# Performance work log

Measured on AMD Instinct MI355X. Metric: run time of the kernel, lower is better.

Reference implementation:

```python
import jax, jax.numpy as jnp
import numpy as np

B, S, H = 4, 1024, 2048
NH, NKV = 32, 8
HD = H // NH  # 64
ROPE_THETA = 10000.0


def setup_inputs() -> dict:
    key = jax.random.key(0)
    ks = jax.random.split(key, 6)
    x = jax.random.normal(ks[0], (B, S, H), dtype=jnp.float32)
    # rotary tables: cos/sin of shape [B, S, HD] (duplicated half-dim layout)
    inv_freq = 1.0 / (ROPE_THETA ** (jnp.arange(0, HD, 2, dtype=jnp.float32) / HD))  # [HD/2]
    t = jnp.arange(S, dtype=jnp.float32)
    freqs = jnp.outer(t, inv_freq)                      # [S, HD/2]
    emb = jnp.concatenate([freqs, freqs], axis=-1)      # [S, HD]
    cos = jnp.broadcast_to(jnp.cos(emb), (B, S, HD))
    sin = jnp.broadcast_to(jnp.sin(emb), (B, S, HD))
    # additive causal mask [B, 1, S, S]
    causal = jnp.where(jnp.arange(S)[:, None] >= jnp.arange(S)[None, :], 0.0, -1e9).astype(jnp.float32)
    attention_mask = jnp.broadcast_to(causal[None, None], (B, 1, S, S))
    scale = 0.02
    Wq = jax.random.normal(ks[1], (H, NH * HD), dtype=jnp.float32) * scale
    Wk = jax.random.normal(ks[2], (H, NKV * HD), dtype=jnp.float32) * scale
    Wv = jax.random.normal(ks[3], (H, NKV * HD), dtype=jnp.float32) * scale
    Wo = jax.random.normal(ks[4], (NH * HD, H), dtype=jnp.float32) * scale
    return {"x": x, "cos": cos, "sin": sin, "attention_mask": attention_mask,
            "Wq": Wq, "Wk": Wk, "Wv": Wv, "Wo": Wo}


def _rotate_half(t):
    h = t.shape[-1] // 2
    return jnp.concatenate([-t[..., h:], t[..., :h]], axis=-1)


def reference(x, cos, sin, attention_mask, Wq, Wk, Wv, Wo):
    b, s, _ = x.shape
    q = (x @ Wq).reshape(b, s, NH, HD).transpose(0, 2, 1, 3)    # [B,NH,S,HD]
    k = (x @ Wk).reshape(b, s, NKV, HD).transpose(0, 2, 1, 3)   # [B,NKV,S,HD]
    v = (x @ Wv).reshape(b, s, NKV, HD).transpose(0, 2, 1, 3)
    c = cos[:, None]  # [B,1,S,HD]
    sn = sin[:, None]
    q = q * c + _rotate_half(q) * sn
    k = k * c + _rotate_half(k) * sn
    n_rep = NH // NKV
    k = jnp.repeat(k, n_rep, axis=1)  # [B,NH,S,HD]
    v = jnp.repeat(v, n_rep, axis=1)
    scaling = HD ** -0.5
    aw = jnp.einsum('bhqd,bhkd->bhqk', q, k) * scaling + attention_mask
    aw = jax.nn.softmax(aw, axis=-1)                            # [B,NH,S,S]
    out = jnp.einsum('bhqk,bhkd->bhqd', aw, v)                  # [B,NH,S,HD]
    out = out.transpose(0, 2, 1, 3).reshape(b, s, NH * HD) @ Wo  # [B,S,H]
    return out, aw
```

## Files before the change

### kernel.cpp

```cpp
#include <hip/hip_runtime.h>
#include <hip/hip_bf16.h>

#define NHQ 32
#define NKV 8
#define SEQ 1024
#define BATCH 4
#define HDIM 2048

typedef short bf16x8 __attribute__((ext_vector_type(8)));
typedef short short4v __attribute__((ext_vector_type(4)));
typedef float f32x4 __attribute__((ext_vector_type(4)));

__device__ __forceinline__ short f2bf(float f) {
  unsigned u = __builtin_bit_cast(unsigned, f);
  u += 0x7fff + ((u >> 16) & 1);
  return (short)(u >> 16);
}
__device__ __forceinline__ float bf2f(short s) {
  unsigned u = ((unsigned)(unsigned short)s) << 16;
  return __builtin_bit_cast(float, u);
}
__device__ __forceinline__ void gl2lds16(const void* g, void* l) {
  __builtin_amdgcn_global_load_lds(
      (const __attribute__((address_space(1))) unsigned int*)g,
      (__attribute__((address_space(3))) unsigned int*)l, 16, 0, 0);
}

__global__ __launch_bounds__(256) void convx_k(
    const float* __restrict__ x, short* __restrict__ xb)
{
  long i = ((long)blockIdx.x * 256 + threadIdx.x) * 4;
  float4 v = *(const float4*)(x + i);
  short4v o = {f2bf(v.x), f2bf(v.y), f2bf(v.z), f2bf(v.w)};
  *(short4v*)(xb + i) = o;
}

__global__ __launch_bounds__(256) void wtrans_k(
    const float* __restrict__ W, short* __restrict__ WT, int K, int N)
{
  __shared__ float t[64][65];
  int k0 = blockIdx.y * 64, n0 = blockIdx.x * 64;
  int r = threadIdx.x >> 4, c = (threadIdx.x & 15) * 4;
#pragma unroll
  for (int it = 0; it < 4; ++it) {
    float4 v = *(const float4*)(W + (long)(k0 + r + it * 16) * N + n0 + c);
    t[c + 0][r + it * 16] = v.x;
    t[c + 1][r + it * 16] = v.y;
    t[c + 2][r + it * 16] = v.z;
    t[c + 3][r + it * 16] = v.w;
  }
  __syncthreads();
  int wr = threadIdx.x >> 2, wc = (threadIdx.x & 3) * 16;
#pragma unroll
  for (int u = 0; u < 4; ++u) {
    short4v o = {f2bf(t[wr][wc + u * 4 + 0]), f2bf(t[wr][wc + u * 4 + 1]),
                 f2bf(t[wr][wc + u * 4 + 2]), f2bf(t[wr][wc + u * 4 + 3])};
    *(short4v*)&WT[(long)(n0 + wr) * K + k0 + wc + u * 4] = o;
  }
}

__global__ __launch_bounds__(256) void gemm_k(
    const short* __restrict__ A, const short* __restrict__ BT,
    void* __restrict__ C, int M, int N, int K, int mode, int nheads)
{
  __shared__ short smA[128 * 32];
  __shared__ short smB[128 * 32];
  const int tid = threadIdx.x;
  const int lane = tid & 63, w = tid >> 6;
  const int wr = w >> 1, wc = w & 1;
  const int lm = lane & 15, lk = lane >> 4;
  const int row0 = blockIdx.y * 128, col0 = blockIdx.x * 128;
  const int c0 = tid, c1 = tid + 256;

  const short* Ab = A + (long)row0 * K;
  const short* Bb = BT + (long)col0 * K;

  f32x4 acc[4][4] = {};

  for (int k0 = 0; k0 < K; k0 += 32) {
    gl2lds16(Ab + (long)(c0 >> 2) * K + k0 + (c0 & 3) * 8, &smA[c0 * 8]);
    gl2lds16(Ab + (long)(c1 >> 2) * K + k0 + (c1 & 3) * 8, &smA[c1 * 8]);
    gl2lds16(Bb + (long)(c0 >> 2) * K + k0 + (c0 & 3) * 8, &smB[c0 * 8]);
    gl2lds16(Bb + (long)(c1 >> 2) * K + k0 + (c1 & 3) * 8, &smB[c1 * 8]);
    __syncthreads();
    bf16x8 af[4], bf[4];
#pragma unroll
    for (int i = 0; i < 4; ++i)
      af[i] = *(const bf16x8*)&smA[(wr * 64 + i * 16 + lm) * 32 + lk * 8];
#pragma unroll
    for (int j = 0; j < 4; ++j)
      bf[j] = *(const bf16x8*)&smB[(wc * 64 + j * 16 + lm) * 32 + lk * 8];
#pragma unroll
    for (int i = 0; i < 4; ++i)
#pragma unroll
      for (int j = 0; j < 4; ++j)
        acc[i][j] = __builtin_amdgcn_mfma_f32_16x16x32_bf16(af[i], bf[j], acc[i][j], 0, 0, 0);
    __syncthreads();
  }

#pragma unroll
  for (int i = 0; i < 4; ++i) {
    int grow = row0 + wr * 64 + i * 16 + lk * 4;
#pragma unroll
    for (int j = 0; j < 4; ++j) {
      int gcol = col0 + wc * 64 + j * 16 + lm;
      if (mode == 0) {
        float* Co = (float*)C;
#pragma unroll
        for (int r = 0; r < 4; ++r)
          Co[(long)(grow + r) * N + gcol] = acc[i][j][r];
      } else if (mode == 1) {
        short* Co = (short*)C;
        int h = gcol >> 6, d = gcol & 63;
#pragma unroll
        for (int r = 0; r < 4; ++r) {
          int row = grow + r;
          int b = row >> 10, s = row & 1023;
          Co[((long)(b * nheads + h) * SEQ + s) * 64 + d] = f2bf(acc[i][j][r]);
        }
      } else {
        short* Co = (short*)C;
        int kvh = gcol >> 6, d = gcol & 63;
        int b = grow >> 10, s0 = grow & 1023;
        short4v o = {f2bf(acc[i][j][0]), f2bf(acc[i][j][1]),
                     f2bf(acc[i][j][2]), f2bf(acc[i][j][3])};
        *(short4v*)&Co[((long)(b * NKV + kvh) * 64 + d) * SEQ + s0] = o;
      }
    }
  }
}

__global__ __launch_bounds__(64) void rope_k(
    short* __restrict__ t, const float* __restrict__ cs,
    const float* __restrict__ sn, int nheads)
{
  long row = blockIdx.x;
  int d = threadIdx.x;
  int s = (int)(row & 1023);
  int b = (int)(row / ((long)nheads << 10));
  float v = bf2f(t[row * 64 + d]);
  float p = __shfl_xor(v, 32);
  float rh = (d < 32) ? -p : p;
  long ci = ((long)(b << 10) + s) * 64 + d;
  t[row * 64 + d] = f2bf(v * cs[ci] + rh * sn[ci]);
}

__global__ __launch_bounds__(256) void fattn_k(
    const short* __restrict__ Qb, const short* __restrict__ Kb,
    const short* __restrict__ Vt, float* __restrict__ aw,
    short* __restrict__ ctxb)
{
  __shared__ short Pl[4][32 * 72];
  const int bh = blockIdx.y;
  const int h = bh & 31, b = bh >> 5;
  const int q0 = blockIdx.x * 128;
  const int tid = threadIdx.x;
  const int lane = tid & 63, wv = tid >> 6;
  const int lm = lane & 15, lk = lane >> 4;

  const short* Qp = Qb + ((long)bh << 16);
  const short* Kp = Kb + ((long)(b * NKV + (h >> 2)) << 16);
  const short* Vp = Vt + ((long)(b * NKV + (h >> 2)) << 16);
  float* awb = aw + ((long)bh << 20);

  const int nch = (q0 >> 6) + 2;
  const int zc = nch * 64;

  if (zc < SEQ) {
    float4 z4 = make_float4(0.f, 0.f, 0.f, 0.f);
    for (int r = wv; r < 128; r += 4)
      for (int c = zc + lane * 4; c < SEQ; c += 256)
        *(float4*)(awb + (long)(q0 + r) * SEQ + c) = z4;
  }

  bf16x8 qa[2][2];
#pragma unroll
  for (int i = 0; i < 2; ++i)
#pragma unroll
    for (int hf = 0; hf < 2; ++hf)
      qa[i][hf] = *(const bf16x8*)(Qp + (long)(q0 + wv * 32 + i * 16 + lm) * 64 + hf * 32 + lk * 8);

  float m[2][4], l[2][4];
#pragma unroll
  for (int i = 0; i < 2; ++i)
#pragma unroll
    for (int r = 0; r < 4; ++r) { m[i][r] = -3.0e38f; l[i][r] = 0.f; }

  for (int ch = 0; ch < nch; ++ch) {
    const int k0c = ch * 64;
    bf16x8 kb[4][2];
#pragma unroll
    for (int j = 0; j < 4; ++j)
#pragma unroll
      for (int hf = 0; hf < 2; ++hf)
        kb[j][hf] = *(const bf16x8*)(Kp + (long)(k0c + j * 16 + lm) * 64 + hf * 32 + lk * 8);
    f32x4 s[2][4] = {};
#pragma unroll
    for (int i = 0; i < 2; ++i)
#pragma unroll
      for (int j = 0; j < 4; ++j) {
        s[i][j] = __builtin_amdgcn_mfma_f32_16x16x32_bf16(qa[i][0], kb[j][0], s[i][j], 0, 0, 0);
        s[i][j] = __builtin_amdgcn_mfma_f32_16x16x32_bf16(qa[i][1], kb[j][1], s[i][j], 0, 0, 0);
      }
#pragma unroll
    for (int i = 0; i < 2; ++i)
#pragma unroll
      for (int r = 0; r < 4; ++r) {
        const int qi = q0 + wv * 32 + i * 16 + lk * 4 + r;
        float cm = -3.0e38f;
#pragma unroll
        for (int j = 0; j < 4; ++j) {
          float sv = s[i][j][r] * 0.125f;
          cm = (qi >= k0c + j * 16 + lm) ? fmaxf(cm, sv) : cm;
        }
#pragma unroll
        for (int off = 1; off <= 8; off <<= 1) cm = fmaxf(cm, __shfl_xor(cm, off));
        float mn = fmaxf(m[i][r], cm);
        float sum = 0.f;
#pragma unroll
        for (int j = 0; j < 4; ++j) {
          float sv = s[i][j][r] * 0.125f;
          sum += (qi >= k0c + j * 16 + lm) ? __expf(sv - mn) : 0.f;
        }
#pragma unroll
        for (int off = 1; off <= 8; off <<= 1) sum += __shfl_xor(sum, off);
        l[i][r] = l[i][r] * __expf(m[i][r] - mn) + sum;
        m[i][r] = mn;
      }
  }
#pragma unroll
  for (int i = 0; i < 2; ++i)
#pragma unroll
    for (int r = 0; r < 4; ++r) l[i][r] = 1.f / l[i][r];

  f32x4 oacc[2][4] = {};
  short* Pw = Pl[wv];
  for (int ch = 0; ch < nch; ++ch) {
    const int k0c = ch * 64;
    bf16x8 kb[4][2];
#pragma unroll
    for (int j = 0; j < 4; ++j)
#pragma unroll
      for (int hf = 0; hf < 2; ++hf)
        kb[j][hf] = *(const bf16x8*)(Kp + (long)(k0c + j * 16 + lm) * 64 + hf * 32 + lk * 8);
    f32x4 s[2][4] = {};
#pragma unroll
    for (int i = 0; i < 2; ++i)
#pragma unroll
      for (int j = 0; j < 4; ++j) {
        s[i][j] = __builtin_amdgcn_mfma_f32_16x16x32_bf16(qa[i][0], kb[j][0], s[i][j], 0, 0, 0);
        s[i][j] = __builtin_amdgcn_mfma_f32_16x16x32_bf16(qa[i][1], kb[j][1], s[i][j], 0, 0, 0);
      }
#pragma unroll
    for (int i = 0; i < 2; ++i)
#pragma unroll
      for (int j = 0; j < 4; ++j)
#pragma unroll
        for (int r = 0; r < 4; ++r) {
          const int qi = q0 + wv * 32 + i * 16 + lk * 4 + r;
          const int ki = k0c + j * 16 + lm;
          float p = (qi >= ki) ? __expf(s[i][j][r] * 0.125f - m[i][r]) * l[i][r] : 0.f;
          awb[(long)qi * SEQ + ki] = p;
          Pw[(i * 16 + lk * 4 + r) * 72 + j * 16 + lm] = f2bf(p);
        }
    __syncthreads();
#pragma unroll
    for (int i = 0; i < 2; ++i) {
      bf16x8 pa0 = *(const bf16x8*)&Pw[(i * 16 + lm) * 72 + lk * 8];
      bf16x8 pa1 = *(const bf16x8*)&Pw[(i * 16 + lm) * 72 + 32 + lk * 8];
#pragma unroll
      for (int dt = 0; dt < 4; ++dt) {
        bf16x8 vb0 = *(const bf16x8*)(Vp + (long)(dt * 16 + lm) * SEQ + k0c + lk * 8);
        bf16x8 vb1 = *(const bf16x8*)(Vp + (long)(dt * 16 + lm) * SEQ + k0c + 32 + lk * 8);
        oacc[i][dt] = __builtin_amdgcn_mfma_f32_16x16x32_bf16(pa0, vb0, oacc[i][dt], 0, 0, 0);
        oacc[i][dt] = __builtin_amdgcn_mfma_f32_16x16x32_bf16(pa1, vb1, oacc[i][dt], 0, 0, 0);
      }
    }
    __syncthreads();
  }

#pragma unroll
  for (int i = 0; i < 2; ++i)
#pragma unroll
    for (int dt = 0; dt < 4; ++dt)
#pragma unroll
      for (int r = 0; r < 4; ++r) {
        int srow = q0 + wv * 32 + i * 16 + lk * 4 + r;
        ctxb[((long)b * SEQ + srow) * HDIM + h * 64 + dt * 16 + lm] = f2bf(oacc[i][dt][r]);
      }
}

extern "C" void kernel_launch(void* const* d_in, const int* in_sizes, int n_in,
                              void* d_out, int out_size, void* d_ws, size_t ws_size,
                              hipStream_t stream) {
  const float* x  = (const float*)d_in[0];
  const float* cs = (const float*)d_in[1];
  const float* sn = (const float*)d_in[2];
  const float* Wq = (const float*)d_in[4];
  const float* Wk = (const float*)d_in[5];
  const float* Wv = (const float*)d_in[6];
  const float* Wo = (const float*)d_in[7];

  float* out = (float*)d_out;
  float* aw  = out + (long)BATCH * SEQ * HDIM;

  short* ws   = (short*)d_ws;
  short* xb   = ws;
  short* WqT  = xb  + (long)4096 * 2048;
  short* WkT  = WqT + (long)2048 * 2048;
  short* WvT  = WkT + (long)512 * 2048;
  short* WoT  = WvT + (long)512 * 2048;
  short* Qb   = WoT + (long)2048 * 2048;
  short* Kb2  = Qb  + (long)BATCH * NHQ * SEQ * 64;
  short* Vt   = Kb2 + (long)BATCH * NKV * SEQ * 64;
  short* ctxb = Vt  + (long)BATCH * NKV * SEQ * 64;

  convx_k<<<(4096 * 2048) / (256 * 4), 256, 0, stream>>>(x, xb);
  wtrans_k<<<dim3(32, 32), 256, 0, stream>>>(Wq, WqT, 2048, 2048);
  wtrans_k<<<dim3(8, 32), 256, 0, stream>>>(Wk, WkT, 2048, 512);
  wtrans_k<<<dim3(8, 32), 256, 0, stream>>>(Wv, WvT, 2048, 512);
  wtrans_k<<<dim3(32, 32), 256, 0, stream>>>(Wo, WoT, 2048, 2048);

  gemm_k<<<dim3(16, 32), 256, 0, stream>>>(xb, WqT, Qb, 4096, 2048, 2048, 1, NHQ);
  gemm_k<<<dim3(4, 32), 256, 0, stream>>>(xb, WkT, Kb2, 4096, 512, 2048, 1, NKV);
  gemm_k<<<dim3(4, 32), 256, 0, stream>>>(xb, WvT, Vt, 4096, 512, 2048, 2, NKV);

  rope_k<<<BATCH * NHQ * SEQ, 64, 0, stream>>>(Qb, cs, sn, NHQ);
  rope_k<<<BATCH * NKV * SEQ, 64, 0, stream>>>(Kb2, cs, sn, NKV);

  fattn_k<<<dim3(8, BATCH * NHQ), 256, 0, stream>>>(Qb, Kb2, Vt, aw, ctxb);

  gemm_k<<<dim3(16, 32), 256, 0, stream>>>(ctxb, WoT, out, 4096, 2048, 2048, 0, 0);
}
```

Baseline: 1.058 ms.

## Fuse QKV projections with RoPE and scaling into one GEMM launch

Merges the Q, K and V projection GEMMs into a single launch over a concatenated weight (WqT, WkT, WvT are contiguous in the workspace), and applies rotary embedding plus the 1/sqrt(d) scale for Q in the GEMM epilogue. The two separate rope kernels and their extra round-trips through global memory go away. In attention, the per-chunk scale multiply is dropped, V fragments are loaded into registers before the MFMAs, and the block-wide __syncthreads are replaced with a per-wave LDS waitcnt, since each wave only uses its own P buffer. The catch is that pre-scaling Q before bf16 rounding changes numerics slightly, and the sync removal relies on per-wave LDS isolation.

```diff
diff --git a/kernel.cpp b/kernel.cpp
--- a/kernel.cpp
+++ b/kernel.cpp
@@ -61,7 +61,8 @@
 
 __global__ __launch_bounds__(256) void gemm_k(
     const short* __restrict__ A, const short* __restrict__ BT,
-    void* __restrict__ C, int M, int N, int K, int mode, int nheads)
+    void* __restrict__ C, int M, int N, int K, int mode,
+    const float* __restrict__ cs, const float* __restrict__ sn)
 {
   __shared__ short smA[128 * 32];
   __shared__ short smB[128 * 32];
@@ -83,66 +84,87 @@
     gl2lds16(Bb + (long)(c0 >> 2) * K + k0 + (c0 & 3) * 8, &smB[c0 * 8]);
     gl2lds16(Bb + (long)(c1 >> 2) * K + k0 + (c1 & 3) * 8, &smB[c1 * 8]);
     __syncthreads();
-    bf16x8 af[4], bf[4];
+    bf16x8 af[4], bfr[4];
 #pragma unroll
     for (int i = 0; i < 4; ++i)
       af[i] = *(const bf16x8*)&smA[(wr * 64 + i * 16 + lm) * 32 + lk * 8];
 #pragma unroll
     for (int j = 0; j < 4; ++j)
-      bf[j] = *(const bf16x8*)&smB[(wc * 64 + j * 16 + lm) * 32 + lk * 8];
+      bfr[j] = *(const bf16x8*)&smB[(wc * 64 + j * 16 + lm) * 32 + lk * 8];
 #pragma unroll
     for (int i = 0; i < 4; ++i)
 #pragma unroll
       for (int j = 0; j < 4; ++j)
-        acc[i][j] = __builtin_amdgcn_mfma_f32_16x16x32_bf16(af[i], bf[j], acc[i][j], 0, 0, 0);
+        acc[i][j] = __builtin_amdgcn_mfma_f32_16x16x32_bf16(af[i], bfr[j], acc[i][j], 0, 0, 0);
     __syncthreads();
   }
 
-#pragma unroll
-  for (int i = 0; i < 4; ++i) {
-    int grow = row0 + wr * 64 + i * 16 + lk * 4;
-#pragma unroll
-    for (int j = 0; j < 4; ++j) {
-      int gcol = col0 + wc * 64 + j * 16 + lm;
-      if (mode == 0) {
-        float* Co = (float*)C;
+  if (mode == 0) {
+    float* Co = (float*)C;
+#pragma unroll
+    for (int i = 0; i < 4; ++i) {
+      int grow = row0 + wr * 64 + i * 16 + lk * 4;
+#pragma unroll
+      for (int j = 0; j < 4; ++j) {
+        int gcol = col0 + wc * 64 + j * 16 + lm;
 #pragma unroll
         for (int r = 0; r < 4; ++r)
           Co[(long)(grow + r) * N + gcol] = acc[i][j][r];
-      } else if (mode == 1) {
-        short* Co = (short*)C;
-        int h = gcol >> 6, d = gcol & 63;
-#pragma unroll
-        for (int r = 0; r < 4; ++r) {
-          int row = grow + r;
-          int b = row >> 10, s = row & 1023;
-          Co[((long)(b * nheads + h) * SEQ + s) * 64 + d] = f2bf(acc[i][j][r]);
-        }
-      } else {
-        short* Co = (short*)C;
-        int kvh = gcol >> 6, d = gcol & 63;
-        int b = grow >> 10, s0 = grow & 1023;
+      }
+    }
+    return;
+  }
+
+  short* Qo = (short*)C;
+  short* Ko = Qo + (long)BATCH * NHQ * SEQ * 64;
+  short* Vo = Ko + (long)BATCH * NKV * SEQ * 64;
+  const int colb = col0 + wc * 64;
+
+  if (colb >= 2560) {
+    const int kvh = (colb - 2560) >> 6;
+#pragma unroll
+    for (int i = 0; i < 4; ++i) {
+      int grow = row0 + wr * 64 + i * 16 + lk * 4;
+      int b = grow >> 10, s0 = grow & 1023;
+#pragma unroll
+      for (int j = 0; j < 4; ++j) {
+        int d = j * 16 + lm;
         short4v o = {f2bf(acc[i][j][0]), f2bf(acc[i][j][1]),
                      f2bf(acc[i][j][2]), f2bf(acc[i][j][3])};
-        *(short4v*)&Co[((long)(b * NKV + kvh) * 64 + d) * SEQ + s0] = o;
-      }
-    }
-  }
-}
-
-__global__ __launch_bounds__(64) void rope_k(
-    short* __restrict__ t, const float* __restrict__ cs,
-    const float* __restrict__ sn, int nheads)
-{
-  long row = blockIdx.x;
-  int d = threadIdx.x;
-  int s = (int)(row & 1023);
-  int b = (int)(row / ((long)nheads << 10));
-  float v = bf2f(t[row * 64 + d]);
-  float p = __shfl_xor(v, 32);
-  float rh = (d < 32) ? -p : p;
-  long ci = ((long)(b << 10) + s) * 64 + d;
-  t[row * 64 + d] = f2bf(v * cs[ci] + rh * sn[ci]);
+        *(short4v*)&Vo[((long)(b * NKV + kvh) * 64 + d) * SEQ + s0] = o;
+      }
+    }
+  } else {
+    const bool isQ = (colb < 2048);
+    short* Co = isQ ? Qo : Ko;
+    const int h = isQ ? (colb >> 6) : ((colb - 2048) >> 6);
+    const int nh = isQ ? NHQ : NKV;
+    const float qs = isQ ? 0.125f : 1.0f;
+#pragma unroll
+    for (int i = 0; i < 4; ++i) {
+      int grow = row0 + wr * 64 + i * 16 + lk * 4;
+      int b = grow >> 10, s = grow & 1023;
+      const float* cb = cs + ((long)(b << 10) + s) * 64;
+      const float* sb = sn + ((long)(b << 10) + s) * 64;
+      short* rowp = Co + ((long)(b * nh + h) * SEQ + s) * 64;
+#pragma unroll
+      for (int r = 0; r < 4; ++r) {
+        float c0 = cb[r * 64 + lm], c1 = cb[r * 64 + lm + 16];
+        float s0 = sb[r * 64 + lm], s1 = sb[r * 64 + lm + 16];
+        float a0 = acc[i][0][r], a1 = acc[i][1][r];
+        float a2 = acc[i][2][r], a3 = acc[i][3][r];
+        float o0 = (a0 * c0 - a2 * s0) * qs;
+        float o1 = (a1 * c1 - a3 * s1) * qs;
+        float o2 = (a2 * c0 + a0 * s0) * qs;
+        float o3 = (a3 * c1 + a1 * s1) * qs;
+        short* rp = rowp + (long)r * 64;
+        rp[lm]      = f2bf(o0);
+        rp[lm + 16] = f2bf(o1);
+        rp[lm + 32] = f2bf(o2);
+        rp[lm + 48] = f2bf(o3);
+      }
+    }
+  }
 }
 
 __global__ __launch_bounds__(256) void fattn_k(
@@ -210,7 +232,7 @@
         float cm = -3.0e38f;
 #pragma unroll
         for (int j = 0; j < 4; ++j) {
-          float sv = s[i][j][r] * 0.125f;
+          float sv = s[i][j][r];
           cm = (qi >= k0c + j * 16 + lm) ? fmaxf(cm, sv) : cm;
         }
 #pragma unroll
@@ -219,7 +241,7 @@
         float sum = 0.f;
 #pragma unroll
         for (int j = 0; j < 4; ++j) {
-          float sv = s[i][j][r] * 0.125f;
+          float sv = s[i][j][r];
           sum += (qi >= k0c + j * 16 + lm) ? __expf(sv - mn) : 0.f;
         }
 #pragma unroll
@@ -259,24 +281,29 @@
         for (int r = 0; r < 4; ++r) {
           const int qi = q0 + wv * 32 + i * 16 + lk * 4 + r;
           const int ki = k0c + j * 16 + lm;
-          float p = (qi >= ki) ? __expf(s[i][j][r] * 0.125f - m[i][r]) * l[i][r] : 0.f;
+          float p = (qi >= ki) ? __expf(s[i][j][r] - m[i][r]) * l[i][r] : 0.f;
           awb[(long)qi * SEQ + ki] = p;
           Pw[(i * 16 + lk * 4 + r) * 72 + j * 16 + lm] = f2bf(p);
         }
-    __syncthreads();
+    asm volatile("s_waitcnt lgkmcnt(0)" ::: "memory");
+    __builtin_amdgcn_sched_barrier(0);
+
+    bf16x8 vb[4][2];
+#pragma unroll
+    for (int dt = 0; dt < 4; ++dt) {
+      vb[dt][0] = *(const bf16x8*)(Vp + (long)(dt * 16 + lm) * SEQ + k0c + lk * 8);
+      vb[dt][1] = *(const bf16x8*)(Vp + (long)(dt * 16 + lm) * SEQ + k0c + 32 + lk * 8);
+    }
 #pragma unroll
     for (int i = 0; i < 2; ++i) {
       bf16x8 pa0 = *(const bf16x8*)&Pw[(i * 16 + lm) * 72 + lk * 8];
       bf16x8 pa1 = *(const bf16x8*)&Pw[(i * 16 + lm) * 72 + 32 + lk * 8];
 #pragma unroll
       for (int dt = 0; dt < 4; ++dt) {
-        bf16x8 vb0 = *(const bf16x8*)(Vp + (long)(dt * 16 + lm) * SEQ + k0c + lk * 8);
-        bf16x8 vb1 = *(const bf16x8*)(Vp + (long)(dt * 16 + lm) * SEQ + k0c + 32 + lk * 8);
-        oacc[i][dt] = __builtin_amdgcn_mfma_f32_16x16x32_bf16(pa0, vb0, oacc[i][dt], 0, 0, 0);
-        oacc[i][dt] = __builtin_amdgcn_mfma_f32_16x16x32_bf16(pa1, vb1, oacc[i][dt], 0, 0, 0);
-      }
-    }
-    __syncthreads();
+        oacc[i][dt] = __builtin_amdgcn_mfma_f32_16x16x32_bf16(pa0, vb[dt][0], oacc[i][dt], 0, 0, 0);
+        oacc[i][dt] = __builtin_amdgcn_mfma_f32_16x16x32_bf16(pa1, vb[dt][1], oacc[i][dt], 0, 0, 0);
+      }
+    }
   }
 
 #pragma unroll
@@ -321,14 +348,9 @@
   wtrans_k<<<dim3(8, 32), 256, 0, stream>>>(Wv, WvT, 2048, 512);
   wtrans_k<<<dim3(32, 32), 256, 0, stream>>>(Wo, WoT, 2048, 2048);
 
-  gemm_k<<<dim3(16, 32), 256, 0, stream>>>(xb, WqT, Qb, 4096, 2048, 2048, 1, NHQ);
-  gemm_k<<<dim3(4, 32), 256, 0, stream>>>(xb, WkT, Kb2, 4096, 512, 2048, 1, NKV);
-  gemm_k<<<dim3(4, 32), 256, 0, stream>>>(xb, WvT, Vt, 4096, 512, 2048, 2, NKV);
-
-  rope_k<<<BATCH * NHQ * SEQ, 64, 0, stream>>>(Qb, cs, sn, NHQ);
-  rope_k<<<BATCH * NKV * SEQ, 64, 0, stream>>>(Kb2, cs, sn, NKV);
+  gemm_k<<<dim3(24, 32), 256, 0, stream>>>(xb, WqT, Qb, 4096, 3072, 2048, 3, cs, sn);
 
   fattn_k<<<dim3(8, BATCH * NHQ), 256, 0, stream>>>(Qb, Kb2, Vt, aw, ctxb);
 
-  gemm_k<<<dim3(16, 32), 256, 0, stream>>>(ctxb, WoT, out, 4096, 2048, 2048, 0, 0);
-}
+  gemm_k<<<dim3(16, 32), 256, 0, stream>>>(ctxb, WoT, out, 4096, 2048, 2048, 0, nullptr, nullptr);
+}
```

Result: faster. 928.6 us (-12.2%).
